# Optimization experiments

Hardware: AMD Instinct MI355X
Metric: run time of the kernel (lower is better)

Reference implementation:

```python
import jax, jax.numpy as jnp
import numpy as np

GROUPS = 8
PAD = 3  # padding = (kernel_size - 1) // 2 with kernel_size = 7


def setup_inputs() -> dict:
    key = jax.random.key(0)
    k0, k1, k2, k3, k4, k5 = jax.random.split(key, 6)
    B, Cin, Cout, H, W, K = 2, 128, 128, 96, 96, 7
    x = jax.random.normal(k0, (B, Cin, H, W), jnp.float32)
    v = jax.random.normal(k1, (B, Cout, H, W), jnp.float32)
    # 1x1 conv weights (kaiming-ish scale), stored as [out, in]
    scale = float(np.sqrt(2.0 / Cout))
    w_q = jax.random.normal(k2, (Cout, Cin), jnp.float32) * scale
    w_k = jax.random.normal(k3, (Cout, Cin), jnp.float32) * scale
    # relative position params: N(0, 1) as in reset_parameters
    rel_h = jax.random.normal(k4, (Cout // 2, 1, 1, K, 1), jnp.float32)
    rel_w = jax.random.normal(k5, (Cout // 2, 1, 1, 1, K), jnp.float32)
    return {"x": x, "v": v, "w_q": w_q, "w_k": w_k, "rel_h": rel_h, "rel_w": rel_w}


def _unfold(t, K, H, W):
    # t: [B, C, H+2P, W+2P] -> [B, C, H, W, K*K] matching torch unfold(2,K,1).unfold(3,K,1) row-major flatten
    return jnp.stack([t[:, :, i:i + H, j:j + W] for i in range(K) for j in range(K)], axis=-1)


def reference(x, v, w_q, w_k, rel_h, rel_w):
    B, Cin, H, W = x.shape
    K = rel_h.shape[3]
    Cout = w_q.shape[0]
    G = GROUPS
    P = PAD

    # 1x1 convs (bias=False); pad-then-conv == conv-then-pad for zero pad, no bias
    q = jnp.einsum('bihw,oi->bohw', x, w_q)            # [B, Cout, H, W]
    kf = jnp.einsum('bihw,oi->bohw', x, w_k)           # [B, Cout, H, W]

    kpad = jnp.pad(kf, ((0, 0), (0, 0), (P, P), (P, P)))
    vpad = jnp.pad(v, ((0, 0), (0, 0), (P, P), (P, P)))

    kk = _unfold(kpad, K, H, W).reshape(B, Cout, H, W, K, K)   # [B,C,H,W,kh,kw]
    vv = _unfold(vpad, K, H, W)                                 # [B,C,H,W,K*K]

    C2 = Cout // 2
    kk = jnp.concatenate([kk[:, :C2] + rel_h, kk[:, C2:] + rel_w], axis=1)
    kk = kk.reshape(B, G, Cout // G, H, W, K * K)
    vv = vv.reshape(B, G, Cout // G, H, W, K * K)
    qq = q.reshape(B, G, Cout // G, H, W, 1)

    attn = jax.nn.softmax(qq * kk, axis=-1)            # per-channel softmax over k*k window
    out = jnp.einsum('bgchwk,bgchwk->bgchw', attn, vv)
    return out.reshape(B, Cout, H, W)
```

## Files before the change

kernel.cpp:

```cpp
#include <hip/hip_runtime.h>
#include <hip/hip_bf16.h>

#define HW 9216
#define CIN 128
#define COUT 128

typedef _Float16 half8 __attribute__((ext_vector_type(8)));
typedef float f32x4 __attribute__((ext_vector_type(4)));

__device__ __forceinline__ float fast_exp2(float x) {
    float r;
    asm("v_exp_f32 %0, %1" : "=v"(r) : "v"(x));
    return r;
}

__device__ __forceinline__ void mfma16(f32x4& d, half8 a, half8 b) {
    asm("v_mfma_f32_16x16x32_f16 %0, %1, %2, %0" : "+v"(d) : "v"(a), "v"(b));
}

__device__ __forceinline__ void gl_lds16(const void* g, void* l) {
    __builtin_amdgcn_global_load_lds(
        (const __attribute__((address_space(1))) unsigned int*)g,
        (__attribute__((address_space(3))) unsigned int*)l, 16, 0, 0);
}

__device__ __forceinline__ unsigned short h_bits(_Float16 h) {
    return __builtin_bit_cast(unsigned short, h);
}

__global__ __launch_bounds__(256) void prep(
    const float* __restrict__ x,
    const float* __restrict__ wq, const float* __restrict__ wk,
    _Float16* __restrict__ xh_t, _Float16* __restrict__ xl_t,
    _Float16* __restrict__ wh_t, _Float16* __restrict__ wl_t)
{
    const int tid = threadIdx.x;
    const int bx = blockIdx.x;
    const int b = blockIdx.y;

    if (bx >= 144) {
        if (b) return;
        int o = (bx - 144) * 32 + (tid >> 3);
        int k0 = (tid & 7) * 16;
        const float* src = (o < 128) ? (wq + o * 128) : (wk + (o - 128) * 128);
        float vals[16];
        #pragma unroll
        for (int t = 0; t < 4; ++t)
            *(float4*)&vals[t * 4] = *(const float4*)&src[k0 + t * 4];
        half8 h0, h1, l0, l1;
        #pragma unroll
        for (int j = 0; j < 8; ++j) {
            _Float16 h = (_Float16)vals[j];
            h0[j] = h; l0[j] = (_Float16)(vals[j] - (float)h);
            _Float16 h2 = (_Float16)vals[j + 8];
            h1[j] = h2; l1[j] = (_Float16)(vals[j + 8] - (float)h2);
        }
        int s = (o & 7) << 3;
        *(half8*)&wh_t[o * 128 + (k0 ^ s)]       = h0;
        *(half8*)&wh_t[o * 128 + ((k0 + 8) ^ s)] = h1;
        *(half8*)&wl_t[o * 128 + (k0 ^ s)]       = l0;
        *(half8*)&wl_t[o * 128 + ((k0 + 8) ^ s)] = l1;
        return;
    }

    __shared__ unsigned int lds[64 * 128];
    const int pixbase = bx * 64;
    const int p = tid & 63;
    const int kw = tid >> 6;
    const float* xb = x + (size_t)b * CIN * HW + pixbase + p;

    #pragma unroll
    for (int i = 0; i < 32; ++i) {
        int k = kw * 32 + i;
        float v = xb[(size_t)k * HW];
        _Float16 h = (_Float16)v;
        _Float16 l = (_Float16)(v - (float)h);
        unsigned int pack = (unsigned int)h_bits(h) | ((unsigned int)h_bits(l) << 16);
        lds[(p * 128 + k) ^ (p & 31)] = pack;
    }
    __syncthreads();

    const int p2 = tid >> 2;
    const int qk = (tid & 3) * 32;
    const int s = (p2 & 7) << 3;
    unsigned int hw_[16], lw_[16];
    #pragma unroll
    for (int i = 0; i < 16; ++i) {
        int pos0 = qk + 2 * i;
        int src0 = pos0 ^ s;
        unsigned int a0 = lds[(p2 * 128 + src0) ^ (p2 & 31)];
        unsigned int a1 = lds[(p2 * 128 + src0 + 1) ^ (p2 & 31)];
        hw_[i] = (a0 & 0xffffu) | (a1 << 16);
        lw_[i] = (a0 >> 16) | (a1 & 0xffff0000u);
    }
    size_t orow = ((size_t)b * HW + pixbase + p2) * 64 + (qk >> 1);
    unsigned int* oh = (unsigned int*)xh_t;
    unsigned int* ol = (unsigned int*)xl_t;
    #pragma unroll
    for (int i = 0; i < 4; ++i) {
        uint4 th = {hw_[i*4], hw_[i*4+1], hw_[i*4+2], hw_[i*4+3]};
        uint4 tl = {lw_[i*4], lw_[i*4+1], lw_[i*4+2], lw_[i*4+3]};
        *(uint4*)&oh[orow + i * 4] = th;
        *(uint4*)&ol[orow + i * 4] = tl;
    }
}

__global__ __launch_bounds__(256) void conv_mfma(
    const _Float16* __restrict__ xh_t, const _Float16* __restrict__ xl_t,
    const _Float16* __restrict__ wh_t, const _Float16* __restrict__ wl_t,
    float* __restrict__ qbuf, float* __restrict__ kbuf)
{
    __shared__ _Float16 xsh[128 * 64];
    __shared__ _Float16 xsl[128 * 64];
    __shared__ _Float16 wsh[128 * 64];
    __shared__ _Float16 wsl[128 * 64];

    const int tid = threadIdx.x;
    const int lane = tid & 63;
    const int wave = tid >> 6;
    const int pixbase = blockIdx.x * 128;
    const int b = blockIdx.y;
    const int half = blockIdx.z;
    const int wbase = half * 128;

    const int wrow = (wave & 1) * 64;
    const int wpix = (wave >> 1) * 64;

    f32x4 acc[4][4];
    #pragma unroll
    for (int m = 0; m < 4; ++m)
        #pragma unroll
        for (int n = 0; n < 4; ++n) { acc[m][n][0]=0.f; acc[m][n][1]=0.f; acc[m][n][2]=0.f; acc[m][n][3]=0.f; }

    const size_t xrow = ((size_t)b * HW + pixbase) * 128;

    #pragma unroll
    for (int kc = 0; kc < 2; ++kc) {
        if (kc) __syncthreads();
        #pragma unroll
        for (int i = 0; i < 4; ++i) {
            int sgl = wave * 4 + i;
            int pix = sgl * 8 + (lane >> 3);
            int j = lane & 7;
            const _Float16* gh = xh_t + xrow + (size_t)pix * 128 + kc * 64 + j * 8;
            const _Float16* gl = xl_t + xrow + (size_t)pix * 128 + kc * 64 + j * 8;
            gl_lds16(gh, (void*)(xsh + sgl * 512));
            gl_lds16(gl, (void*)(xsl + sgl * 512));
        }
        #pragma unroll
        for (int i = 0; i < 4; ++i) {
            int sgl = wave * 4 + i;
            int o = sgl * 8 + (lane >> 3);
            int j = lane & 7;
            const _Float16* gh = wh_t + (size_t)(wbase + o) * 128 + kc * 64 + j * 8;
            const _Float16* gl = wl_t + (size_t)(wbase + o) * 128 + kc * 64 + j * 8;
            gl_lds16(gh, (void*)(wsh + sgl * 512));
            gl_lds16(gl, (void*)(wsl + sgl * 512));
        }
        __syncthreads();

        #pragma unroll
        for (int ks = 0; ks < 2; ++ks) {
            const int kb = ks * 32 + (lane >> 4) * 8;
            half8 ah[4], al[4];
            #pragma unroll
            for (int m = 0; m < 4; ++m) {
                int o = wrow + m * 16 + (lane & 15);
                int idx = (o * 64 + kb) ^ ((o & 7) << 3);
                ah[m] = *(const half8*)&wsh[idx];
                al[m] = *(const half8*)&wsl[idx];
            }
            #pragma unroll
            for (int n = 0; n < 4; ++n) {
                int p = wpix + n * 16 + (lane & 15);
                int idx = (p * 64 + kb) ^ ((p & 7) << 3);
                half8 bh = *(const half8*)&xsh[idx];
                half8 bl = *(const half8*)&xsl[idx];
                #pragma unroll
                for (int m = 0; m < 4; ++m) {
                    mfma16(acc[m][n], ah[m], bh);
                    mfma16(acc[m][n], al[m], bh);
                    mfma16(acc[m][n], ah[m], bl);
                }
            }
        }
    }

    asm volatile("s_nop 7\n\ts_nop 7"
        : "+v"(acc[0][0]), "+v"(acc[0][1]), "+v"(acc[0][2]), "+v"(acc[0][3]),
          "+v"(acc[1][0]), "+v"(acc[1][1]), "+v"(acc[1][2]), "+v"(acc[1][3]),
          "+v"(acc[2][0]), "+v"(acc[2][1]), "+v"(acc[2][2]), "+v"(acc[2][3]),
          "+v"(acc[3][0]), "+v"(acc[3][1]), "+v"(acc[3][2]), "+v"(acc[3][3]));

    float* obuf = half ? kbuf : qbuf;
    #pragma unroll
    for (int m = 0; m < 4; ++m) {
        #pragma unroll
        for (int n = 0; n < 4; ++n) {
            int pc = pixbase + wpix + n * 16 + (lane & 15);
            #pragma unroll
            for (int r = 0; r < 4; ++r) {
                int row = wrow + m * 16 + (lane >> 4) * 4 + r;
                obuf[((size_t)b * COUT + row) * HW + pc] = acc[m][n][r];
            }
        }
    }
}

__global__ __launch_bounds__(192) void attn_v7(
    const float* __restrict__ qbuf,
    const float* __restrict__ kbuf,
    const float* __restrict__ v,
    const float* __restrict__ rel_h,
    const float* __restrict__ rel_w,
    float* __restrict__ out)
{
    __shared__ __align__(16) float ks[22 * 108];
    __shared__ __align__(16) float vs[22 * 108];

    const int tid = threadIdx.x;
    const int th = blockIdx.x * 16;
    const int bc = blockIdx.y;
    const int c = bc & 127;

    const float* kp = kbuf + (size_t)bc * HW;
    const float* vp = v    + (size_t)bc * HW;

    for (int idx = tid; idx < 22 * 102; idx += 192) {
        int r = idx / 102, cl = idx - r * 102;
        int gr = th - 3 + r, gc = cl - 3;
        bool ok = ((unsigned)gr < 96u) && ((unsigned)gc < 96u);
        float kv = ok ? kp[gr * 96 + gc] : 0.f;
        float vv = ok ? vp[gr * 96 + gc] : 0.f;
        ks[r * 108 + cl] = kv;
        vs[r * 108 + cl] = vv;
    }

    const bool is_h = (c < 64);
    const float* rbase = is_h ? (rel_h + c * 7) : (rel_w + (c - 64) * 7);
    float r7[7];
    #pragma unroll
    for (int i = 0; i < 7; ++i) r7[i] = rbase[i];

    const int ty = tid / 12;
    const int tx = tid - ty * 12;

    const float* qrow = qbuf + (size_t)bc * HW + (th + ty) * 96 + tx * 8;
    float4 qa = *(const float4*)qrow;
    float4 qb = *(const float4*)(qrow + 4);
    const float L2E = 1.4426950408889634f;
    float q2[8] = {qa.x * L2E, qa.y * L2E, qa.z * L2E, qa.w * L2E,
                   qb.x * L2E, qb.y * L2E, qb.z * L2E, qb.w * L2E};

    float s[8], a[8];
    #pragma unroll
    for (int j = 0; j < 8; ++j) { s[j] = 0.f; a[j] = 0.f; }

    __syncthreads();

    const float* krow = &ks[ty * 108 + tx * 8];
    const float* vrow = &vs[ty * 108 + tx * 8];

    #pragma unroll
    for (int dh = 0; dh < 7; ++dh) {
        float kr[16], vr[16];
        #pragma unroll
        for (int t = 0; t < 4; ++t) {
            *(float4*)&kr[t * 4] = *(const float4*)&krow[dh * 108 + t * 4];
            *(float4*)&vr[t * 4] = *(const float4*)&vrow[dh * 108 + t * 4];
        }

        if (is_h) {
            float rh = r7[dh];
            #pragma unroll
            for (int j = 0; j < 8; ++j) {
                float qr = q2[j] * rh;
                #pragma unroll
                for (int dw = 0; dw < 7; ++dw) {
                    float e = fast_exp2(fmaf(q2[j], kr[j + dw], qr));
                    s[j] += e;
                    a[j] = fmaf(e, vr[j + dw], a[j]);
                }
            }
        } else {
            #pragma unroll
            for (int j = 0; j < 8; ++j) {
                #pragma unroll
                for (int dw = 0; dw < 7; ++dw) {
                    float e = fast_exp2(q2[j] * (kr[j + dw] + r7[dw]));
                    s[j] += e;
                    a[j] = fmaf(e, vr[j + dw], a[j]);
                }
            }
        }
    }

    float* orow = out + (size_t)bc * HW + (th + ty) * 96 + tx * 8;
    float4 o0, o1;
    o0.x = a[0] * __builtin_amdgcn_rcpf(s[0]);
    o0.y = a[1] * __builtin_amdgcn_rcpf(s[1]);
    o0.z = a[2] * __builtin_amdgcn_rcpf(s[2]);
    o0.w = a[3] * __builtin_amdgcn_rcpf(s[3]);
    o1.x = a[4] * __builtin_amdgcn_rcpf(s[4]);
    o1.y = a[5] * __builtin_amdgcn_rcpf(s[5]);
    o1.z = a[6] * __builtin_amdgcn_rcpf(s[6]);
    o1.w = a[7] * __builtin_amdgcn_rcpf(s[7]);
    *(float4*)orow = o0;
    *(float4*)(orow + 4) = o1;
}

extern "C" void kernel_launch(void* const* d_in, const int* in_sizes, int n_in,
                              void* d_out, int out_size, void* d_ws, size_t ws_size,
                              hipStream_t stream) {
    const float* x  = (const float*)d_in[0];
    const float* v  = (const float*)d_in[1];
    const float* wq = (const float*)d_in[2];
    const float* wk = (const float*)d_in[3];
    const float* rh = (const float*)d_in[4];
    const float* rw = (const float*)d_in[5];
    float* out = (float*)d_out;

    float* qbuf = (float*)d_ws;
    float* kbuf = qbuf + (size_t)2 * COUT * HW;
    _Float16* xh = (_Float16*)(kbuf + (size_t)2 * COUT * HW);
    _Float16* xl = xh + (size_t)2 * HW * 128;
    _Float16* wh = xl + (size_t)2 * HW * 128;
    _Float16* wl = wh + 256 * 128;

    prep<<<dim3(152, 2), 256, 0, stream>>>(x, wq, wk, xh, xl, wh, wl);
    conv_mfma<<<dim3(72, 2, 2), 256, 0, stream>>>(xh, xl, wh, wl, qbuf, kbuf);
    attn_v7<<<dim3(6, 256), 192, 0, stream>>>(qbuf, kbuf, v, rh, rw, out);
}
```

Baseline: 51.51 us.

## Retile attention into 32x32 2D tiles with 4 pixels per thread

Switches the attention kernel from 16-row full-width strips with 8 pixels per thread to 32x32 square tiles with 256 threads each computing 4 pixels. It also precomputes q*rel_w products so the rel_w branch uses one fma per exponent. The aim is better occupancy and less per-thread register pressure. The cost is more LDS reads per output and a slightly different halo overhead.

```diff
diff --git a/kernel.cpp b/kernel.cpp
--- a/kernel.cpp
+++ b/kernel.cpp
@@ -207,7 +207,7 @@
     }
 }
 
-__global__ __launch_bounds__(192) void attn_v7(
+__global__ __launch_bounds__(256) void attn_v8(
     const float* __restrict__ qbuf,
     const float* __restrict__ kbuf,
     const float* __restrict__ v,
@@ -215,25 +215,25 @@
     const float* __restrict__ rel_w,
     float* __restrict__ out)
 {
-    __shared__ __align__(16) float ks[22 * 108];
-    __shared__ __align__(16) float vs[22 * 108];
+    __shared__ __align__(16) float ks[38 * 40];
+    __shared__ __align__(16) float vs[38 * 40];
 
     const int tid = threadIdx.x;
-    const int th = blockIdx.x * 16;
+    const int tile = blockIdx.x;
     const int bc = blockIdx.y;
     const int c = bc & 127;
+    const int tw = (tile % 3) * 32;
+    const int th = (tile / 3) * 32;
 
     const float* kp = kbuf + (size_t)bc * HW;
     const float* vp = v    + (size_t)bc * HW;
 
-    for (int idx = tid; idx < 22 * 102; idx += 192) {
-        int r = idx / 102, cl = idx - r * 102;
-        int gr = th - 3 + r, gc = cl - 3;
+    for (int idx = tid; idx < 38 * 38; idx += 256) {
+        int r = idx / 38, cl = idx - r * 38;
+        int gr = th - 3 + r, gc = tw - 3 + cl;
         bool ok = ((unsigned)gr < 96u) && ((unsigned)gc < 96u);
-        float kv = ok ? kp[gr * 96 + gc] : 0.f;
-        float vv = ok ? vp[gr * 96 + gc] : 0.f;
-        ks[r * 108 + cl] = kv;
-        vs[r * 108 + cl] = vv;
+        ks[r * 40 + cl] = ok ? kp[gr * 96 + gc] : 0.f;
+        vs[r * 40 + cl] = ok ? vp[gr * 96 + gc] : 0.f;
     }
 
     const bool is_h = (c < 64);
@@ -242,38 +242,41 @@
     #pragma unroll
     for (int i = 0; i < 7; ++i) r7[i] = rbase[i];
 
-    const int ty = tid / 12;
-    const int tx = tid - ty * 12;
-
-    const float* qrow = qbuf + (size_t)bc * HW + (th + ty) * 96 + tx * 8;
+    const int ty = tid >> 3;
+    const int tx = tid & 7;
+
+    const float* qrow = qbuf + (size_t)bc * HW + (th + ty) * 96 + tw + tx * 4;
     float4 qa = *(const float4*)qrow;
-    float4 qb = *(const float4*)(qrow + 4);
     const float L2E = 1.4426950408889634f;
-    float q2[8] = {qa.x * L2E, qa.y * L2E, qa.z * L2E, qa.w * L2E,
-                   qb.x * L2E, qb.y * L2E, qb.z * L2E, qb.w * L2E};
-
-    float s[8], a[8];
-    #pragma unroll
-    for (int j = 0; j < 8; ++j) { s[j] = 0.f; a[j] = 0.f; }
+    float q2[4] = {qa.x * L2E, qa.y * L2E, qa.z * L2E, qa.w * L2E};
+
+    float qr7[28];
+    #pragma unroll
+    for (int j = 0; j < 4; ++j)
+        #pragma unroll
+        for (int dw = 0; dw < 7; ++dw) qr7[j * 7 + dw] = q2[j] * r7[dw];
+
+    float s[4] = {0.f, 0.f, 0.f, 0.f};
+    float a[4] = {0.f, 0.f, 0.f, 0.f};
 
     __syncthreads();
 
-    const float* krow = &ks[ty * 108 + tx * 8];
-    const float* vrow = &vs[ty * 108 + tx * 8];
+    const float* kb0 = &ks[ty * 40 + tx * 4];
+    const float* vb0 = &vs[ty * 40 + tx * 4];
 
     #pragma unroll
     for (int dh = 0; dh < 7; ++dh) {
-        float kr[16], vr[16];
-        #pragma unroll
-        for (int t = 0; t < 4; ++t) {
-            *(float4*)&kr[t * 4] = *(const float4*)&krow[dh * 108 + t * 4];
-            *(float4*)&vr[t * 4] = *(const float4*)&vrow[dh * 108 + t * 4];
+        float kr[12], vr[12];
+        #pragma unroll
+        for (int t = 0; t < 3; ++t) {
+            *(float4*)&kr[t * 4] = *(const float4*)&kb0[dh * 40 + t * 4];
+            *(float4*)&vr[t * 4] = *(const float4*)&vb0[dh * 40 + t * 4];
         }
 
         if (is_h) {
             float rh = r7[dh];
             #pragma unroll
-            for (int j = 0; j < 8; ++j) {
+            for (int j = 0; j < 4; ++j) {
                 float qr = q2[j] * rh;
                 #pragma unroll
                 for (int dw = 0; dw < 7; ++dw) {
@@ -284,10 +287,10 @@
             }
         } else {
             #pragma unroll
-            for (int j = 0; j < 8; ++j) {
+            for (int j = 0; j < 4; ++j) {
                 #pragma unroll
                 for (int dw = 0; dw < 7; ++dw) {
-                    float e = fast_exp2(q2[j] * (kr[j + dw] + r7[dw]));
+                    float e = fast_exp2(fmaf(q2[j], kr[j + dw], qr7[j * 7 + dw]));
                     s[j] += e;
                     a[j] = fmaf(e, vr[j + dw], a[j]);
                 }
@@ -295,18 +298,13 @@
         }
     }
 
-    float* orow = out + (size_t)bc * HW + (th + ty) * 96 + tx * 8;
-    float4 o0, o1;
-    o0.x = a[0] * __builtin_amdgcn_rcpf(s[0]);
-    o0.y = a[1] * __builtin_amdgcn_rcpf(s[1]);
-    o0.z = a[2] * __builtin_amdgcn_rcpf(s[2]);
-    o0.w = a[3] * __builtin_amdgcn_rcpf(s[3]);
-    o1.x = a[4] * __builtin_amdgcn_rcpf(s[4]);
-    o1.y = a[5] * __builtin_amdgcn_rcpf(s[5]);
-    o1.z = a[6] * __builtin_amdgcn_rcpf(s[6]);
-    o1.w = a[7] * __builtin_amdgcn_rcpf(s[7]);
-    *(float4*)orow = o0;
-    *(float4*)(orow + 4) = o1;
+    float* orow = out + (size_t)bc * HW + (th + ty) * 96 + tw + tx * 4;
+    float4 o4;
+    o4.x = a[0] * __builtin_amdgcn_rcpf(s[0]);
+    o4.y = a[1] * __builtin_amdgcn_rcpf(s[1]);
+    o4.z = a[2] * __builtin_amdgcn_rcpf(s[2]);
+    o4.w = a[3] * __builtin_amdgcn_rcpf(s[3]);
+    *(float4*)orow = o4;
 }
 
 extern "C" void kernel_launch(void* const* d_in, const int* in_sizes, int n_in,
@@ -329,5 +327,5 @@
 
     prep<<<dim3(152, 2), 256, 0, stream>>>(x, wq, wk, xh, xl, wh, wl);
     conv_mfma<<<dim3(72, 2, 2), 256, 0, stream>>>(xh, xl, wh, wl, qbuf, kbuf);
-    attn_v7<<<dim3(6, 256), 192, 0, stream>>>(qbuf, kbuf, v, rh, rw, out);
-}
+    attn_v8<<<dim3(9, 256), 256, 0, stream>>>(qbuf, kbuf, v, rh, rw, out);
+}
```

Measured after the change: 48.40 us. 1.06x faster.
